# Performance work log

Hardware: AMD Instinct MI355X
Metric: run time of the kernel (lower is better)

Reference implementation:

```python
import jax, jax.numpy as jnp
import numpy as np

N = {'QENT': 20000, 'CENT': 50000, 'SPAN': 40000, 'SENT': 40000}
E = 250000
IN_DIM, HID = 256, 128
NEG_SLOPE = 0.2  # GATConv default negative_slope
RELS = [('QENT', 'SPAN'), ('QENT', 'SENT'), ('CENT', 'SENT'), ('SPAN', 'CENT'), ('CENT', 'CENT')]
ENAMES = ['e_qent_span', 'e_qent_sent', 'e_cent_sent', 'e_span_cent', 'e_cent_cooccur']


def setup_inputs() -> dict:
    key = jax.random.key(0)
    ks = jax.random.split(key, 20)
    inp = {}
    for i, t in enumerate(['QENT', 'CENT', 'SPAN', 'SENT']):
        inp['x_' + t] = jax.random.normal(ks[i], (N[t], IN_DIM), jnp.float32)
    for i, (nm, (s, d)) in enumerate(zip(ENAMES, RELS)):
        k1, k2 = jax.random.split(ks[4 + i])
        src = jax.random.randint(k1, (E,), 0, N[s])
        dst = jax.random.randint(k2, (E,), 0, N[d])
        inp[nm] = jnp.stack([src, dst]).astype(jnp.int32)
    inp['lin_W'] = jax.random.normal(ks[10], (4, IN_DIM, HID), jnp.float32) / np.sqrt(IN_DIM).astype(np.float32)
    inp['lin_b'] = jnp.zeros((4, HID), jnp.float32)
    inp['conv_Ws'] = jax.random.normal(ks[11], (2, 5, HID, HID), jnp.float32) / np.sqrt(HID).astype(np.float32)
    inp['conv_Wd'] = jax.random.normal(ks[12], (2, 5, HID, HID), jnp.float32) / np.sqrt(HID).astype(np.float32)
    inp['conv_as'] = jax.random.normal(ks[13], (2, 5, HID), jnp.float32) / np.sqrt(HID).astype(np.float32)
    inp['conv_ad'] = jax.random.normal(ks[14], (2, 5, HID), jnp.float32) / np.sqrt(HID).astype(np.float32)
    inp['conv_b'] = jnp.zeros((2, 5, HID), jnp.float32)
    inp['out_W'] = jax.random.normal(ks[15], (HID, 1), jnp.float32) / np.sqrt(HID).astype(np.float32)
    inp['out_b'] = jnp.zeros((1,), jnp.float32)
    return inp


def _gat(x_src, x_dst, edge, Ws, Wd, a_s, a_d, b, n_dst):
    """PyG GATConv, heads=1, concat=True, add_self_loops=False, bipartite lin_src/lin_dst."""
    hs = x_src @ Ws                       # [Ns, H]
    hd = x_dst @ Wd                       # [Nd, H]
    src, dst = edge[0], edge[1]
    e = jax.nn.leaky_relu((hs @ a_s)[src] + (hd @ a_d)[dst], NEG_SLOPE)  # [E]
    m = jax.ops.segment_max(e, dst, num_segments=n_dst)
    m = jnp.where(jnp.isfinite(m), m, 0.0)
    ex = jnp.exp(e - m[dst])
    denom = jax.ops.segment_sum(ex, dst, num_segments=n_dst)
    alpha = ex / (denom[dst] + 1e-16)     # segment softmax (PyG adds 1e-16)
    out = jax.ops.segment_sum(alpha[:, None] * hs[src], dst, num_segments=n_dst)
    return out + b


def _forward(x_QENT, x_CENT, x_SPAN, x_SENT,
             e_qent_span, e_qent_sent, e_cent_sent, e_span_cent, e_cent_cooccur,
             lin_W, lin_b, conv_Ws, conv_Wd, conv_as, conv_ad, conv_b, out_W, out_b):
    # per-type input projection (pyg Linear has bias)
    x = {'QENT': x_QENT @ lin_W[0] + lin_b[0],
         'CENT': x_CENT @ lin_W[1] + lin_b[1],
         'SPAN': x_SPAN @ lin_W[2] + lin_b[2],
         'SENT': x_SENT @ lin_W[3] + lin_b[3]}
    for l in range(2):
        p = lambda r: (conv_Ws[l, r], conv_Wd[l, r], conv_as[l, r], conv_ad[l, r], conv_b[l, r])
        span = _gat(x['QENT'], x['SPAN'], e_qent_span, *p(0), N['SPAN'])
        sent = (_gat(x['QENT'], x['SENT'], e_qent_sent, *p(1), N['SENT'])
                + _gat(x['CENT'], x['SENT'], e_cent_sent, *p(2), N['SENT']))  # HeteroConv aggr='sum'
        cent = (_gat(x['SPAN'], x['CENT'], e_span_cent, *p(3), N['CENT'])
                + _gat(x['CENT'], x['CENT'], e_cent_cooccur, *p(4), N['CENT']))
        x = {'QENT': x['QENT'],  # QENT has no incoming edges; carried through so layer 2 can use it as source
             'SPAN': jax.nn.relu(span),
             'SENT': jax.nn.relu(sent),
             'CENT': jax.nn.relu(cent)}
    return (x['SPAN'] @ out_W + out_b)[:, 0]  # squeeze(-1) -> [N_SPAN]


def reference(x_QENT, x_CENT, x_SPAN, x_SENT,
              e_qent_span, e_qent_sent, e_cent_sent, e_span_cent, e_cent_cooccur,
              lin_W, lin_b, conv_Ws, conv_Wd, conv_as, conv_ad, conv_b, out_W, out_b):
    return _forward(x_QENT, x_CENT, x_SPAN, x_SENT,
                    e_qent_span, e_qent_sent, e_cent_sent, e_span_cent, e_cent_cooccur,
                    lin_W, lin_b, conv_Ws, conv_Wd, conv_as, conv_ad, conv_b, out_W, out_b)
```

## Files before the change

kernel.cpp:

```cpp
#include <hip/hip_runtime.h>
#include <hip/hip_fp16.h>

#define IN_DIM 256
#define HID 128
#define ELLW 16
#define OVF_CAP 32768

using bf16x8 = __attribute__((ext_vector_type(8))) short;
using f32x4 = __attribute__((ext_vector_type(4))) float;

struct h8 { __half2 a, b, c, d; };

__device__ __forceinline__ unsigned short f2bf(float f) {
    unsigned u = __float_as_uint(f);
    u += 0x7fffu + ((u >> 16) & 1u);
    return (unsigned short)(u >> 16);
}

template <int CTRL>
__device__ __forceinline__ float dpp_rot(float x) {
    return __int_as_float(
        __builtin_amdgcn_update_dpp(0, __float_as_int(x), CTRL, 0xf, 0xf, false));
}
__device__ __forceinline__ float rsum16(float x) {
    x += dpp_rot<0x121>(x);
    x += dpp_rot<0x122>(x);
    x += dpp_rot<0x124>(x);
    x += dpp_rot<0x128>(x);
    return x;
}
__device__ __forceinline__ float rmax16(float x) {
    x = fmaxf(x, dpp_rot<0x121>(x));
    x = fmaxf(x, dpp_rot<0x122>(x));
    x = fmaxf(x, dpp_rot<0x124>(x));
    x = fmaxf(x, dpp_rot<0x128>(x));
    return x;
}

__device__ __forceinline__ float lrelu(float t) { return t > 0.f ? t : 0.2f * t; }

__device__ __forceinline__ void accum8(f32x4& a0, f32x4& a1, float a, const h8& hv) {
    const float2 f0 = __half22float2(hv.a);
    const float2 f1 = __half22float2(hv.b);
    const float2 f2 = __half22float2(hv.c);
    const float2 f3 = __half22float2(hv.d);
    a0[0] += a * f0.x; a0[1] += a * f0.y;
    a0[2] += a * f1.x; a0[3] += a * f1.y;
    a1[0] += a * f2.x; a1[1] += a * f2.y;
    a1[2] += a * f3.x; a1[3] += a * f3.y;
}

__device__ __forceinline__ float epilogue16(const f32x4& a0, const f32x4& a1,
                                            const float* __restrict__ bias,
                                            const float* __restrict__ dvec, int sl) {
    const f32x4 bb0 = *reinterpret_cast<const f32x4*>(bias + sl * 8);
    const f32x4 bb1 = *reinterpret_cast<const f32x4*>(bias + sl * 8 + 4);
    const f32x4 d0 = *reinterpret_cast<const f32x4*>(dvec + sl * 8);
    const f32x4 d1 = *reinterpret_cast<const f32x4*>(dvec + sl * 8 + 4);
    float q = 0.f;
#pragma unroll
    for (int i = 0; i < 4; ++i) {
        q += fmaxf(a0[i] + bb0[i], 0.f) * d0[i];
        q += fmaxf(a1[i] + bb1[i], 0.f) * d1[i];
    }
    return rsum16(q);
}

__global__ __launch_bounds__(256) void setup_k(const float* __restrict__ lin_W,
                                               const float* __restrict__ lin_b,
                                               const float* __restrict__ conv_Ws,
                                               const float* __restrict__ Wd,
                                               const float* __restrict__ adv,
                                               short* __restrict__ wt0,
                                               short* __restrict__ wt1,
                                               float* __restrict__ bc,
                                               float* __restrict__ wd_out,
                                               float* __restrict__ v2,
                                               float* __restrict__ c2,
                                               int* __restrict__ deg,
                                               int* __restrict__ ovf_cnt, int NS) {
    const int b = blockIdx.x;
    if (b < 256) {
        const int idx = b * 256 + threadIdx.x;
        const int l = idx >> 15;
        const int rem = idx & 32767;
        const int k = rem >> 7;
        const int n = rem & 127;
        const float* lw = lin_W + (size_t)k * HID;
        const float* cw = conv_Ws + (size_t)(l * 5) * HID * HID + n;
        float s = 0.f;
#pragma unroll 4
        for (int m = 0; m < HID; ++m) s += lw[m] * cw[(size_t)m * HID];
        short* wt = l ? wt1 : wt0;
        wt[((k >> 3) << 10) + (n << 3) + (k & 7)] = (short)f2bf(s);
    } else if (b == 256) {
        const int t = threadIdx.x;
        const int l = t >> 7;
        const int n = t & 127;
        const float* cw = conv_Ws + (size_t)(l * 5) * HID * HID + n;
        float s = 0.f;
#pragma unroll 4
        for (int m = 0; m < HID; ++m) s += lin_b[m] * cw[(size_t)m * HID];
        bc[t] = s;
        if (t == 0) ovf_cnt[0] = 0;
    } else if (b == 257) {
        __shared__ float wd1s[HID];
        const int t = threadIdx.x;
        const int l = t >> 7, j = t & 127;
        const float* w = Wd + ((size_t)(l * 5) * HID + j) * HID;
        const float* a = adv + (size_t)(l * 5) * HID;
        float s = 0.f;
        for (int k = 0; k < HID; k += 4) {
            const float4 wv = *reinterpret_cast<const float4*>(w + k);
            const float4 av = *reinterpret_cast<const float4*>(a + k);
            s += wv.x * av.x + wv.y * av.y + wv.z * av.z + wv.w * av.w;
        }
        wd_out[t] = s;
        if (l == 0) wd1s[j] = s;
        __syncthreads();
        const float* wr = lin_W + 2 * (size_t)IN_DIM * HID + (size_t)t * HID;
        float p = 0.f;
        for (int k = 0; k < HID; k += 4) {
            const float4 wv = *reinterpret_cast<const float4*>(wr + k);
            p += wv.x * wd1s[k] + wv.y * wd1s[k + 1] + wv.z * wd1s[k + 2] +
                 wv.w * wd1s[k + 3];
        }
        v2[t] = p;
        if (t == 0) {
            const float* br = lin_b + 2 * HID;
            float q = 0.f;
            for (int k = 0; k < HID; ++k) q += br[k] * wd1s[k];
            c2[0] = q;
        }
    } else {
        const int i4 = ((b - 258) * 256 + threadIdx.x) * 4;
        if (i4 + 4 <= NS) {
            *reinterpret_cast<int4*>(deg + i4) = make_int4(0, 0, 0, 0);
        } else {
            for (int i = i4; i < NS; ++i) deg[i] = 0;
        }
    }
}

__global__ __launch_bounds__(256) void build_gemm_k(
    const int* __restrict__ src, const int* __restrict__ dst, int E,
    int* __restrict__ deg, int* __restrict__ ell, int2* __restrict__ ovf,
    int* __restrict__ ovf_cnt, const float* __restrict__ A,
    const short* __restrict__ Wt0, const short* __restrict__ Wt1,
    const float* __restrict__ bc, __half* __restrict__ hs,
    float* __restrict__ as12,
    const float* __restrict__ a1v, const float* __restrict__ a2v, int N,
    const float* __restrict__ x_span, const float* __restrict__ v2,
    const float* __restrict__ c2, float* __restrict__ ad1_out, int NS, int gb2,
    int ab) {
    const int b = (int)blockIdx.x;
    if (b < gb2) {
        const int l = b & 1;
        const int bid = b >> 1;
        const short* Wt = l ? Wt1 : Wt0;
        const float* av = l ? a2v : a1v;
        const int tid = threadIdx.x;
        const int w = tid >> 6;
        const int lane = tid & 63;
        const int m16 = lane & 15;
        const int kg = lane >> 4;

        const int arow = bid * 64 + w * 16 + m16;
        const bool ok = arow < N;

        f32x4 acc[8];
#pragma unroll
        for (int j = 0; j < 8; ++j) acc[j] = (f32x4){0.f, 0.f, 0.f, 0.f};

        for (int k0 = 0; k0 < IN_DIM; k0 += 32) {
            bf16x8 af = {0, 0, 0, 0, 0, 0, 0, 0};
            if (ok) {
                const float* ap = A + (size_t)arow * IN_DIM + k0 + kg * 8;
                const float4 f0 = *reinterpret_cast<const float4*>(ap);
                const float4 f1 = *reinterpret_cast<const float4*>(ap + 4);
                af[0] = (short)f2bf(f0.x); af[1] = (short)f2bf(f0.y);
                af[2] = (short)f2bf(f0.z); af[3] = (short)f2bf(f0.w);
                af[4] = (short)f2bf(f1.x); af[5] = (short)f2bf(f1.y);
                af[6] = (short)f2bf(f1.z); af[7] = (short)f2bf(f1.w);
            }
            const short* bbase = Wt + (((k0 >> 3) + kg) << 10);
#pragma unroll
            for (int j = 0; j < 8; ++j) {
                const bf16x8 bf =
                    *reinterpret_cast<const bf16x8*>(bbase + ((j * 16 + m16) << 3));
                acc[j] = __builtin_amdgcn_mfma_f32_16x16x32_bf16(af, bf, acc[j], 0, 0, 0);
            }
        }

        const int rbase = bid * 64 + w * 16 + kg * 4;
        float p[4] = {0.f, 0.f, 0.f, 0.f};
#pragma unroll
        for (int j = 0; j < 8; ++j) {
            const int col = j * 16 + m16;
            const float bv = bc[l * 128 + col];
            const float a = av[col];
            const int so = j * 32 + ((m16 >> 3) << 4) + (m16 & 7) + l * 8;
#pragma unroll
            for (int r = 0; r < 4; ++r) {
                const int row = rbase + r;
                const float v = acc[j][r] + bv;
                if (row < N) hs[(size_t)row * 256 + so] = __float2half(v);
                p[r] += v * a;
            }
        }
#pragma unroll
        for (int r = 0; r < 4; ++r) p[r] = rsum16(p[r]);
        if (m16 == 0)
#pragma unroll
            for (int r = 0; r < 4; ++r) {
                const int row = rbase + r;
                if (row < N) as12[2 * (size_t)row + l] = p[r];
            }
        return;
    }
    if (b < gb2 + ab) {
        const int idx = (b - gb2) * 256 + threadIdx.x;
        const int row = idx >> 4;
        const int sl = threadIdx.x & 15;
        if (row >= NS) return;
        const float* xr = x_span + (size_t)row * IN_DIM + sl * 16;
        const float* vr = v2 + sl * 16;
        float p = 0.f;
#pragma unroll
        for (int i = 0; i < 4; ++i) {
            const float4 xv = *reinterpret_cast<const float4*>(xr + i * 4);
            const float4 vv = *reinterpret_cast<const float4*>(vr + i * 4);
            p += xv.x * vv.x + xv.y * vv.y + xv.z * vv.z + xv.w * vv.w;
        }
        p = rsum16(p);
        if (sl == 0) ad1_out[row] = p + c2[0];
        return;
    }
    const int e = (b - gb2 - ab) * 256 + threadIdx.x;
    if (e < E) {
        const int d = dst[e], s = src[e];
        const int pos = atomicAdd(deg + d, 1);
        if (pos < ELLW) {
            ell[(size_t)d * ELLW + pos] = s;
        } else {
            const int oi = atomicAdd(ovf_cnt, 1);
            if (oi < OVF_CAP) ovf[oi] = make_int2(d, s);
        }
    }
}

__global__ __launch_bounds__(256, 4) void gat_fused_k(
    const int* __restrict__ deg_arr, const int* __restrict__ ell,
    const int2* __restrict__ ovf, const int* __restrict__ ovf_cnt_p,
    const float* __restrict__ ad1_arr, const float2* __restrict__ as12,
    const __half* __restrict__ hs, const float* __restrict__ b1,
    const float* __restrict__ wd2v, const float* __restrict__ b2,
    const float* __restrict__ outW, const float* __restrict__ outb,
    float* __restrict__ out, int Ndst) {
    const int row = (blockIdx.x * blockDim.x + threadIdx.x) >> 6;
    const int lane = threadIdx.x & 63;
    const int sl = lane & 15;
    const int eg = lane >> 4;
    if (row >= Ndst) return;

    const int deg = deg_arr[row];
    int ce = ell[(size_t)row * ELLW + sl];
    if (sl >= deg) ce = 0;
    const float2 asv = as12[ce];
    const float ad1 = ad1_arr[row];

    if (deg <= ELLW) {
        const float ex1 = (sl < deg) ? __expf(lrelu(asv.x + ad1)) : 0.f;
        const float al1 = ex1 / (rsum16(ex1) + 1e-16f);

        f32x4 a0 = {0.f, 0.f, 0.f, 0.f}, a1 = {0.f, 0.f, 0.f, 0.f};
        h8 h2s[4];
#pragma unroll
        for (int r = 0; r < 4; ++r) {
            if (r * 4 < deg) {
                const int e = r * 4 + eg;
                const int s = __shfl(ce, e, 64);
                const float a = __shfl(al1, e, 64);
                const __half* hb = hs + (size_t)s * 256 + sl * 16;
                const h8 hv1 = *reinterpret_cast<const h8*>(hb);
                h2s[r] = *reinterpret_cast<const h8*>(hb + 8);
                accum8(a0, a1, a, hv1);
            }
        }
#pragma unroll
        for (int i = 0; i < 4; ++i) {
            a0[i] += __shfl_xor(a0[i], 16, 64);
            a0[i] += __shfl_xor(a0[i], 32, 64);
            a1[i] += __shfl_xor(a1[i], 16, 64);
            a1[i] += __shfl_xor(a1[i], 32, 64);
        }
        const float ad2 = epilogue16(a0, a1, b1, wd2v, sl);

        const float ex2 = (sl < deg) ? __expf(lrelu(asv.y + ad2)) : 0.f;
        const float al2 = ex2 / (rsum16(ex2) + 1e-16f);

        f32x4 b0 = {0.f, 0.f, 0.f, 0.f}, b1v = {0.f, 0.f, 0.f, 0.f};
#pragma unroll
        for (int r = 0; r < 4; ++r) {
            if (r * 4 < deg) {
                const float a = __shfl(al2, r * 4 + eg, 64);
                accum8(b0, b1v, a, h2s[r]);
            }
        }
#pragma unroll
        for (int i = 0; i < 4; ++i) {
            b0[i] += __shfl_xor(b0[i], 16, 64);
            b0[i] += __shfl_xor(b0[i], 32, 64);
            b1v[i] += __shfl_xor(b1v[i], 16, 64);
            b1v[i] += __shfl_xor(b1v[i], 32, 64);
        }
        const float q = epilogue16(b0, b1v, b2, outW, sl);
        if (lane == 0) out[row] = q + outb[0];
    } else {
        int oc = *ovf_cnt_p;
        if (oc > OVF_CAP) oc = OVF_CAP;
        float ad = ad1;
#pragma unroll
        for (int layer = 0; layer < 2; ++layer) {
            const float ac = layer ? asv.y : asv.x;
            const int ho = layer ? 8 : 0;
            const float* bias = layer ? b2 : b1;
            const float* dvec = layer ? outW : wd2v;

            float te = lrelu(ac + ad);
            float m = rmax16(te);
            for (int i = 0; i < oc; ++i) {
                const int2 o = ovf[i];
                if (o.x == row) {
                    const float2 oas = as12[o.y];
                    m = fmaxf(m, lrelu((layer ? oas.y : oas.x) + ad));
                }
            }
            const float ex = __expf(te - m);
            float dsum = rsum16(ex);
            for (int i = 0; i < oc; ++i) {
                const int2 o = ovf[i];
                if (o.x == row) {
                    const float2 oas = as12[o.y];
                    dsum += __expf(lrelu((layer ? oas.y : oas.x) + ad) - m);
                }
            }
            const float inv = 1.f / (dsum + 1e-16f);
            const float al = ex * inv;

            f32x4 acc0 = {0.f, 0.f, 0.f, 0.f}, acc1 = {0.f, 0.f, 0.f, 0.f};
            for (int i = 0; i < 16; ++i) {
                const int s = __shfl(ce, i, 64);
                float a = __shfl(al, i, 64);
                if (eg != 0) a = 0.f;
                const h8 hv =
                    *reinterpret_cast<const h8*>(hs + (size_t)s * 256 + sl * 16 + ho);
                accum8(acc0, acc1, a, hv);
            }
            for (int i = 0; i < oc; ++i) {
                const int2 o = ovf[i];
                if (o.x == row && eg == 0) {
                    const float2 oas = as12[o.y];
                    const float a = __expf(lrelu((layer ? oas.y : oas.x) + ad) - m) * inv;
                    const h8 hv =
                        *reinterpret_cast<const h8*>(hs + (size_t)o.y * 256 + sl * 16 + ho);
                    accum8(acc0, acc1, a, hv);
                }
            }
#pragma unroll
            for (int i = 0; i < 4; ++i) {
                acc0[i] += __shfl_xor(acc0[i], 16, 64);
                acc0[i] += __shfl_xor(acc0[i], 32, 64);
                acc1[i] += __shfl_xor(acc1[i], 16, 64);
                acc1[i] += __shfl_xor(acc1[i], 32, 64);
            }
            const float q = epilogue16(acc0, acc1, bias, dvec, sl);
            if (layer == 0) {
                ad = q;
            } else if (lane == 0) {
                out[row] = q + outb[0];
            }
        }
    }
}

extern "C" void kernel_launch(void* const* d_in, const int* in_sizes, int n_in,
                              void* d_out, int out_size, void* d_ws, size_t ws_size,
                              hipStream_t stream) {
    const float* x_qent = (const float*)d_in[0];
    const float* x_span = (const float*)d_in[2];
    const int* e_qs = (const int*)d_in[4];
    const float* lin_W = (const float*)d_in[9];
    const float* lin_b = (const float*)d_in[10];
    const float* conv_Ws = (const float*)d_in[11];
    const float* conv_Wd = (const float*)d_in[12];
    const float* conv_as = (const float*)d_in[13];
    const float* conv_ad = (const float*)d_in[14];
    const float* conv_b = (const float*)d_in[15];
    const float* out_W = (const float*)d_in[16];
    const float* out_b = (const float*)d_in[17];

    const int NQ = in_sizes[0] / IN_DIM;
    const int NS = in_sizes[2] / IN_DIM;
    const int E = in_sizes[4] / 2;
    const int* srcp = e_qs;
    const int* dstp = e_qs + E;
    (void)n_in; (void)out_size;

    float* ws = (float*)d_ws;
    size_t off = 0;
    auto alloc = [&](size_t n) {
        n = (n + 3) & ~(size_t)3;
        float* p = ws + off;
        off += n;
        return p;
    };
    __half* hs = (__half*)alloc((size_t)NQ * 128);
    float* as12 = alloc(2 * (size_t)NQ);
    float* ad1 = alloc(NS);
    float* wd2 = alloc(2 * HID);
    float* v2 = alloc(IN_DIM);
    float* c2 = alloc(1);
    float* bc = alloc(2 * HID);
    int* deg = (int*)alloc(NS);
    int* ell = (int*)alloc((size_t)NS * ELLW);
    int2* ovf = (int2*)alloc(2 * OVF_CAP);
    int* ovf_cnt = (int*)alloc(1);
    short* wt0 = (short*)alloc(IN_DIM * HID / 2);
    short* wt1 = (short*)alloc(IN_DIM * HID / 2);
    (void)ws_size;

    const int zd = (NS + 1023) / 1024;
    setup_k<<<dim3(258 + zd), dim3(256), 0, stream>>>(
        lin_W, lin_b, conv_Ws, conv_Wd, conv_ad, wt0, wt1, bc, wd2, v2, c2, deg, ovf_cnt,
        NS);

    const int gb2 = 2 * ((NQ + 63) / 64);
    const int ab = ((size_t)NS * 16 + 255) / 256;
    const int eb = (E + 255) / 256;
    build_gemm_k<<<dim3(gb2 + ab + eb), dim3(256), 0, stream>>>(
        srcp, dstp, E, deg, ell, ovf, ovf_cnt, x_qent, wt0, wt1, bc, hs, as12, conv_as,
        conv_as + 5 * (size_t)HID, NQ, x_span, v2, c2, ad1, NS, gb2, ab);

    gat_fused_k<<<dim3(((size_t)NS * 64 + 255) / 256), dim3(256), 0, stream>>>(
        deg, ell, ovf, ovf_cnt, ad1, (const float2*)as12, hs, conv_b, wd2 + HID,
        conv_b + 5 * (size_t)HID, out_W, out_b, (float*)d_out, NS);
}
```

Before: 81.60 us.

## Split GEMM from edge build, prefetch A rows, zero ELL to drop degree guards

The fused build/GEMM kernel becomes a dedicated GEMM kernel that preloads every A row for the whole K range into registers before the MFMA loop, plus a separate kernel for ELL construction and the ad1 dot products. The setup kernel now also zero-fills the ELL table, so the aggregation kernel can drop its per-slot degree checks and always gather four edge groups, reading row 0 for empty slots with zero weight. The GAT kernel's launch-bounds occupancy hint drops from 4 to 3. This trades an extra launch, a larger zero-fill and wasted gathers on low-degree rows for better memory-level parallelism and less branching.

```diff
diff --git a/kernel.cpp b/kernel.cpp
--- a/kernel.cpp
+++ b/kernel.cpp
@@ -78,7 +78,8 @@
                                                float* __restrict__ v2,
                                                float* __restrict__ c2,
                                                int* __restrict__ deg,
-                                               int* __restrict__ ovf_cnt, int NS) {
+                                               int* __restrict__ ell,
+                                               int* __restrict__ ovf_cnt, int NS, int zd) {
     const int b = blockIdx.x;
     if (b < 256) {
         const int idx = b * 256 + threadIdx.x;
@@ -132,94 +133,114 @@
             for (int k = 0; k < HID; ++k) q += br[k] * wd1s[k];
             c2[0] = q;
         }
-    } else {
+    } else if (b < 258 + zd) {
         const int i4 = ((b - 258) * 256 + threadIdx.x) * 4;
         if (i4 + 4 <= NS) {
             *reinterpret_cast<int4*>(deg + i4) = make_int4(0, 0, 0, 0);
         } else {
             for (int i = i4; i < NS; ++i) deg[i] = 0;
         }
-    }
-}
-
-__global__ __launch_bounds__(256) void build_gemm_k(
-    const int* __restrict__ src, const int* __restrict__ dst, int E,
-    int* __restrict__ deg, int* __restrict__ ell, int2* __restrict__ ovf,
-    int* __restrict__ ovf_cnt, const float* __restrict__ A,
-    const short* __restrict__ Wt0, const short* __restrict__ Wt1,
-    const float* __restrict__ bc, __half* __restrict__ hs,
-    float* __restrict__ as12,
-    const float* __restrict__ a1v, const float* __restrict__ a2v, int N,
-    const float* __restrict__ x_span, const float* __restrict__ v2,
-    const float* __restrict__ c2, float* __restrict__ ad1_out, int NS, int gb2,
-    int ab) {
+    } else {
+        const int total = NS * ELLW;
+        const int i4 = ((b - 258 - zd) * 256 + threadIdx.x) * 4;
+        if (i4 + 4 <= total) *reinterpret_cast<int4*>(ell + i4) = make_int4(0, 0, 0, 0);
+    }
+}
+
+__global__ __launch_bounds__(256, 2) void gemm_k(const float* __restrict__ A,
+                                                 const short* __restrict__ Wt0,
+                                                 const short* __restrict__ Wt1,
+                                                 const float* __restrict__ bc,
+                                                 __half* __restrict__ hs,
+                                                 float* __restrict__ as12,
+                                                 const float* __restrict__ a1v,
+                                                 const float* __restrict__ a2v, int N) {
+    const int l = blockIdx.x & 1;
+    const int bid = blockIdx.x >> 1;
+    const short* Wt = l ? Wt1 : Wt0;
+    const float* av = l ? a2v : a1v;
+    const int tid = threadIdx.x;
+    const int w = tid >> 6;
+    const int lane = tid & 63;
+    const int m16 = lane & 15;
+    const int kg = lane >> 4;
+
+    const int arow = bid * 64 + w * 16 + m16;
+    const bool ok = arow < N;
+
+    float4 a_reg[16];
+    if (ok) {
+        const float* ap = A + (size_t)arow * IN_DIM + kg * 8;
+#pragma unroll
+        for (int kk = 0; kk < 8; ++kk) {
+            a_reg[2 * kk] = *reinterpret_cast<const float4*>(ap + kk * 32);
+            a_reg[2 * kk + 1] = *reinterpret_cast<const float4*>(ap + kk * 32 + 4);
+        }
+    } else {
+#pragma unroll
+        for (int i = 0; i < 16; ++i) a_reg[i] = make_float4(0.f, 0.f, 0.f, 0.f);
+    }
+    __builtin_amdgcn_sched_barrier(0);
+
+    f32x4 acc[8];
+#pragma unroll
+    for (int j = 0; j < 8; ++j) acc[j] = (f32x4){0.f, 0.f, 0.f, 0.f};
+
+#pragma unroll
+    for (int kk = 0; kk < 8; ++kk) {
+        const float4 f0 = a_reg[2 * kk];
+        const float4 f1 = a_reg[2 * kk + 1];
+        bf16x8 af;
+        af[0] = (short)f2bf(f0.x); af[1] = (short)f2bf(f0.y);
+        af[2] = (short)f2bf(f0.z); af[3] = (short)f2bf(f0.w);
+        af[4] = (short)f2bf(f1.x); af[5] = (short)f2bf(f1.y);
+        af[6] = (short)f2bf(f1.z); af[7] = (short)f2bf(f1.w);
+        const short* bbase = Wt + (((kk << 2) + kg) << 10);
+#pragma unroll
+        for (int j = 0; j < 8; ++j) {
+            const bf16x8 bf = *reinterpret_cast<const bf16x8*>(bbase + ((j * 16 + m16) << 3));
+            acc[j] = __builtin_amdgcn_mfma_f32_16x16x32_bf16(af, bf, acc[j], 0, 0, 0);
+        }
+    }
+
+    const int rbase = bid * 64 + w * 16 + kg * 4;
+    float p[4] = {0.f, 0.f, 0.f, 0.f};
+#pragma unroll
+    for (int j = 0; j < 8; ++j) {
+        const int col = j * 16 + m16;
+        const float bv = bc[l * 128 + col];
+        const float a = av[col];
+        const int so = j * 32 + ((m16 >> 3) << 4) + (m16 & 7) + l * 8;
+#pragma unroll
+        for (int r = 0; r < 4; ++r) {
+            const int row = rbase + r;
+            const float v = acc[j][r] + bv;
+            if (row < N) hs[(size_t)row * 256 + so] = __float2half(v);
+            p[r] += v * a;
+        }
+    }
+#pragma unroll
+    for (int r = 0; r < 4; ++r) p[r] = rsum16(p[r]);
+    if (m16 == 0)
+#pragma unroll
+        for (int r = 0; r < 4; ++r) {
+            const int row = rbase + r;
+            if (row < N) as12[2 * (size_t)row + l] = p[r];
+        }
+}
+
+__global__ __launch_bounds__(256) void misc_k(const int* __restrict__ src,
+                                              const int* __restrict__ dst, int E,
+                                              int* __restrict__ deg, int* __restrict__ ell,
+                                              int2* __restrict__ ovf,
+                                              int* __restrict__ ovf_cnt,
+                                              const float* __restrict__ x_span,
+                                              const float* __restrict__ v2,
+                                              const float* __restrict__ c2,
+                                              float* __restrict__ ad1_out, int NS, int ab) {
     const int b = (int)blockIdx.x;
-    if (b < gb2) {
-        const int l = b & 1;
-        const int bid = b >> 1;
-        const short* Wt = l ? Wt1 : Wt0;
-        const float* av = l ? a2v : a1v;
-        const int tid = threadIdx.x;
-        const int w = tid >> 6;
-        const int lane = tid & 63;
-        const int m16 = lane & 15;
-        const int kg = lane >> 4;
-
-        const int arow = bid * 64 + w * 16 + m16;
-        const bool ok = arow < N;
-
-        f32x4 acc[8];
-#pragma unroll
-        for (int j = 0; j < 8; ++j) acc[j] = (f32x4){0.f, 0.f, 0.f, 0.f};
-
-        for (int k0 = 0; k0 < IN_DIM; k0 += 32) {
-            bf16x8 af = {0, 0, 0, 0, 0, 0, 0, 0};
-            if (ok) {
-                const float* ap = A + (size_t)arow * IN_DIM + k0 + kg * 8;
-                const float4 f0 = *reinterpret_cast<const float4*>(ap);
-                const float4 f1 = *reinterpret_cast<const float4*>(ap + 4);
-                af[0] = (short)f2bf(f0.x); af[1] = (short)f2bf(f0.y);
-                af[2] = (short)f2bf(f0.z); af[3] = (short)f2bf(f0.w);
-                af[4] = (short)f2bf(f1.x); af[5] = (short)f2bf(f1.y);
-                af[6] = (short)f2bf(f1.z); af[7] = (short)f2bf(f1.w);
-            }
-            const short* bbase = Wt + (((k0 >> 3) + kg) << 10);
-#pragma unroll
-            for (int j = 0; j < 8; ++j) {
-                const bf16x8 bf =
-                    *reinterpret_cast<const bf16x8*>(bbase + ((j * 16 + m16) << 3));
-                acc[j] = __builtin_amdgcn_mfma_f32_16x16x32_bf16(af, bf, acc[j], 0, 0, 0);
-            }
-        }
-
-        const int rbase = bid * 64 + w * 16 + kg * 4;
-        float p[4] = {0.f, 0.f, 0.f, 0.f};
-#pragma unroll
-        for (int j = 0; j < 8; ++j) {
-            const int col = j * 16 + m16;
-            const float bv = bc[l * 128 + col];
-            const float a = av[col];
-            const int so = j * 32 + ((m16 >> 3) << 4) + (m16 & 7) + l * 8;
-#pragma unroll
-            for (int r = 0; r < 4; ++r) {
-                const int row = rbase + r;
-                const float v = acc[j][r] + bv;
-                if (row < N) hs[(size_t)row * 256 + so] = __float2half(v);
-                p[r] += v * a;
-            }
-        }
-#pragma unroll
-        for (int r = 0; r < 4; ++r) p[r] = rsum16(p[r]);
-        if (m16 == 0)
-#pragma unroll
-            for (int r = 0; r < 4; ++r) {
-                const int row = rbase + r;
-                if (row < N) as12[2 * (size_t)row + l] = p[r];
-            }
-        return;
-    }
-    if (b < gb2 + ab) {
-        const int idx = (b - gb2) * 256 + threadIdx.x;
+    if (b < ab) {
+        const int idx = b * 256 + threadIdx.x;
         const int row = idx >> 4;
         const int sl = threadIdx.x & 15;
         if (row >= NS) return;
@@ -236,7 +257,7 @@
         if (sl == 0) ad1_out[row] = p + c2[0];
         return;
     }
-    const int e = (b - gb2 - ab) * 256 + threadIdx.x;
+    const int e = (b - ab) * 256 + threadIdx.x;
     if (e < E) {
         const int d = dst[e], s = src[e];
         const int pos = atomicAdd(deg + d, 1);
@@ -249,7 +270,7 @@
     }
 }
 
-__global__ __launch_bounds__(256, 4) void gat_fused_k(
+__global__ __launch_bounds__(256, 3) void gat_fused_k(
     const int* __restrict__ deg_arr, const int* __restrict__ ell,
     const int2* __restrict__ ovf, const int* __restrict__ ovf_cnt_p,
     const float* __restrict__ ad1_arr, const float2* __restrict__ as12,
@@ -264,10 +285,9 @@
     if (row >= Ndst) return;
 
     const int deg = deg_arr[row];
-    int ce = ell[(size_t)row * ELLW + sl];
-    if (sl >= deg) ce = 0;
+    const int ce = ell[(size_t)row * ELLW + sl];
+    const float ad1 = ad1_arr[row];
     const float2 asv = as12[ce];
-    const float ad1 = ad1_arr[row];
 
     if (deg <= ELLW) {
         const float ex1 = (sl < deg) ? __expf(lrelu(asv.x + ad1)) : 0.f;
@@ -277,15 +297,13 @@
         h8 h2s[4];
 #pragma unroll
         for (int r = 0; r < 4; ++r) {
-            if (r * 4 < deg) {
-                const int e = r * 4 + eg;
-                const int s = __shfl(ce, e, 64);
-                const float a = __shfl(al1, e, 64);
-                const __half* hb = hs + (size_t)s * 256 + sl * 16;
-                const h8 hv1 = *reinterpret_cast<const h8*>(hb);
-                h2s[r] = *reinterpret_cast<const h8*>(hb + 8);
-                accum8(a0, a1, a, hv1);
-            }
+            const int e = r * 4 + eg;
+            const int s = __shfl(ce, e, 64);
+            const float a = __shfl(al1, e, 64);
+            const __half* hb = hs + (size_t)s * 256 + sl * 16;
+            const h8 hv1 = *reinterpret_cast<const h8*>(hb);
+            h2s[r] = *reinterpret_cast<const h8*>(hb + 8);
+            accum8(a0, a1, a, hv1);
         }
 #pragma unroll
         for (int i = 0; i < 4; ++i) {
@@ -302,10 +320,8 @@
         f32x4 b0 = {0.f, 0.f, 0.f, 0.f}, b1v = {0.f, 0.f, 0.f, 0.f};
 #pragma unroll
         for (int r = 0; r < 4; ++r) {
-            if (r * 4 < deg) {
-                const float a = __shfl(al2, r * 4 + eg, 64);
-                accum8(b0, b1v, a, h2s[r]);
-            }
+            const float a = __shfl(al2, r * 4 + eg, 64);
+            accum8(b0, b1v, a, h2s[r]);
         }
 #pragma unroll
         for (int i = 0; i < 4; ++i) {
@@ -431,16 +447,19 @@
     (void)ws_size;
 
     const int zd = (NS + 1023) / 1024;
-    setup_k<<<dim3(258 + zd), dim3(256), 0, stream>>>(
-        lin_W, lin_b, conv_Ws, conv_Wd, conv_ad, wt0, wt1, bc, wd2, v2, c2, deg, ovf_cnt,
-        NS);
+    const int ze = (NS * ELLW + 1023) / 1024;
+    setup_k<<<dim3(258 + zd + ze), dim3(256), 0, stream>>>(
+        lin_W, lin_b, conv_Ws, conv_Wd, conv_ad, wt0, wt1, bc, wd2, v2, c2, deg, ell,
+        ovf_cnt, NS, zd);
 
     const int gb2 = 2 * ((NQ + 63) / 64);
+    gemm_k<<<dim3(gb2), dim3(256), 0, stream>>>(x_qent, wt0, wt1, bc, hs, as12, conv_as,
+                                                conv_as + 5 * (size_t)HID, NQ);
+
     const int ab = ((size_t)NS * 16 + 255) / 256;
     const int eb = (E + 255) / 256;
-    build_gemm_k<<<dim3(gb2 + ab + eb), dim3(256), 0, stream>>>(
-        srcp, dstp, E, deg, ell, ovf, ovf_cnt, x_qent, wt0, wt1, bc, hs, as12, conv_as,
-        conv_as + 5 * (size_t)HID, NQ, x_span, v2, c2, ad1, NS, gb2, ab);
+    misc_k<<<dim3(ab + eb), dim3(256), 0, stream>>>(srcp, dstp, E, deg, ell, ovf, ovf_cnt,
+                                                    x_span, v2, c2, ad1, NS, ab);
 
     gat_fused_k<<<dim3(((size_t)NS * 64 + 255) / 256), dim3(256), 0, stream>>>(
         deg, ell, ovf, ovf_cnt, ad1, (const float2*)as12, hs, conv_b, wd2 + HID,
```

Result: slower. 93.47 us (+14.5%).
